# Optimization experiments

Hardware: AMD Instinct MI355X
Metric: run time of the kernel (lower is better)

Reference implementation:

```python
import jax, jax.numpy as jnp
import numpy as np
from jax import lax

WINDOW_SIZE = 11
SIGMA = 1.5
DATA_RANGE = 1.0


def _gaussian_window(channels):
    coords = jnp.arange(WINDOW_SIZE, dtype=jnp.float32) - WINDOW_SIZE // 2
    g = jnp.exp(-coords ** 2 / (2.0 * SIGMA ** 2))
    g = g / g.sum()
    w2d = jnp.outer(g, g)
    w2d = w2d / w2d.sum()
    # depthwise kernel: (C, 1, K, K) in OIHW with feature_group_count=C
    return jnp.broadcast_to(w2d, (channels, 1, WINDOW_SIZE, WINDOW_SIZE))


def _dwconv(x, window, channels):
    pad = WINDOW_SIZE // 2
    return lax.conv_general_dilated(
        x, window,
        window_strides=(1, 1),
        padding=[(pad, pad), (pad, pad)],
        dimension_numbers=('NCHW', 'OIHW', 'NCHW'),
        feature_group_count=channels,
    )


def setup_inputs() -> dict:
    key = jax.random.key(0)
    k1, k2 = jax.random.split(key)
    B, C, H, W = 16, 3, 512, 512
    x = jax.random.uniform(k1, (B, C, H, W), dtype=jnp.float32)
    y = jax.random.uniform(k2, (B, C, H, W), dtype=jnp.float32)
    return {"x": x, "y": y}


def reference(x, y):
    channels = x.shape[1]
    window = _gaussian_window(channels)
    mu_x = _dwconv(x, window, channels)
    mu_y = _dwconv(y, window, channels)
    mu_x2 = mu_x * mu_x
    mu_y2 = mu_y * mu_y
    mu_xy = mu_x * mu_y
    sigma_x2 = _dwconv(x * x, window, channels) - mu_x2
    sigma_y2 = _dwconv(y * y, window, channels) - mu_y2
    sigma_xy = _dwconv(x * y, window, channels) - mu_xy
    c1 = (0.01 * DATA_RANGE) ** 2
    c2 = (0.03 * DATA_RANGE) ** 2
    ssim_map = (2 * mu_xy + c1) * (2 * sigma_xy + c2) / (
        (mu_x2 + mu_y2 + c1) * (sigma_x2 + sigma_y2 + c2) + 1e-08)
    per_image = ssim_map.mean(axis=(1, 2, 3))
    return 1.0 - per_image.mean()
```

## Files before the change

kernel.cpp:

```cpp
#include <hip/hip_runtime.h>
#include <math.h>


#define IMG_W 512
#define IMG_H 512
#define PLANES 48
#define TX 64
#define TY 32
#define RAD 5
#define KW 11
#define NPAIR 21
#define SJ 65
#define NT 256
#define GDX (IMG_W / TX)
#define GDY (IMG_H / TY)
#define NBLK (GDX * GDY * PLANES)

typedef _Float16 h2 __attribute__((ext_vector_type(2)));

#if __has_builtin(__builtin_amdgcn_fdot2)
__device__ __forceinline__ float DOT2(h2 a, h2 b, float c) {
    return __builtin_amdgcn_fdot2(a, b, c, false);
}
#else
__device__ __forceinline__ float DOT2(h2 a, h2 b, float c) {
    return c + (float)a.x * (float)b.x + (float)a.y * (float)b.y;
}
#endif

__device__ __forceinline__ h2 pkrtz(float a, float b) {
    auto t = __builtin_amdgcn_cvt_pkrtz(a, b);
    h2 r;
    __builtin_memcpy(&r, &t, sizeof(r));
    return r;
}

template<bool INTERIOR>
__device__ __forceinline__ void hpass_item(
    int r, int g, int ty0, int bx0,
    const float* __restrict__ xp, const float* __restrict__ yp,
    _Float16* __restrict__ hbh,
    const h2 (* __restrict__ w2)[6])
{
    const int gy = ty0 + r;
    const int j0 = bx0 + g * 8;
    const float4 z4 = make_float4(0.f, 0.f, 0.f, 0.f);

    h2 xh[11], yh[11];
    {
        const bool rowok = INTERIOR || ((unsigned)gy < (unsigned)IMG_H);
        const float* rowx = xp + (size_t)gy * IMG_W;
        const float* rowy = yp + (size_t)gy * IMG_W;
        #pragma unroll
        for (int v = 0; v < 6; ++v) {
            const int gx = j0 - 8 + 4 * v;
            float4 xa, ya;
            if (rowok && (INTERIOR || ((unsigned)gx < (unsigned)IMG_W))) {
                xa = *(const float4*)(rowx + gx);
                ya = *(const float4*)(rowy + gx);
            } else { xa = z4; ya = z4; }
            if (v > 0) {
                xh[2*v] = pkrtz(xa.x, xa.y);
                yh[2*v] = pkrtz(ya.x, ya.y);
            }
            if (v < 5 || true) {
                if (2*v + 1 <= 10) {
                    xh[2*v+1] = pkrtz(xa.z, xa.w);
                    yh[2*v+1] = pkrtz(ya.z, ya.w);
                }
            }
        }
    }

    const int pp = r >> 1, rr = r & 1;
    _Float16* base = hbh + ((pp * 5) * SJ + g * 8) * 2 + rr;
    const int pstr = SJ * 2;

    #pragma unroll
    for (int u = 0; u < 8; ++u) {
        const int t0 = (u + 3) >> 1;
        const h2* wt = w2[(u & 1) ^ 1];
        float fX = 0.f, fY = 0.f;
        #pragma unroll
        for (int q = 0; q < 6; ++q) {
            fX = DOT2(xh[t0 + q], wt[q], fX);
            fY = DOT2(yh[t0 + q], wt[q], fY);
        }
        base[2*u + 0*pstr] = (_Float16)fX;
        base[2*u + 1*pstr] = (_Float16)fY;
    }

    h2 xxh[11], yyh[11], xyh[11];
    #pragma unroll
    for (int t = 1; t <= 10; ++t) {
        xxh[t] = xh[t] * xh[t];
        yyh[t] = yh[t] * yh[t];
        xyh[t] = xh[t] * yh[t];
    }

    #pragma unroll
    for (int u = 0; u < 8; ++u) {
        const int t0 = (u + 3) >> 1;
        const h2* wt = w2[(u & 1) ^ 1];
        float fXX = 0.f, fYY = 0.f, fXY = 0.f;
        #pragma unroll
        for (int q = 0; q < 6; ++q) {
            fXX = DOT2(xxh[t0 + q], wt[q], fXX);
            fYY = DOT2(yyh[t0 + q], wt[q], fYY);
            fXY = DOT2(xyh[t0 + q], wt[q], fXY);
        }
        base[2*u + 2*pstr] = (_Float16)fXX;
        base[2*u + 3*pstr] = (_Float16)fYY;
        base[2*u + 4*pstr] = (_Float16)fXY;
    }
}

__global__ __launch_bounds__(NT, 4) void ssim_tile_kernel(
    const float* __restrict__ x, const float* __restrict__ y,
    float* __restrict__ partials)
{
    __shared__ h2 hb[NPAIR][5][SJ];
    __shared__ float wave_sums[NT / 64];

    float w[KW];
    {
        float s = 0.f;
        #pragma unroll
        for (int k = 0; k < KW; ++k) {
            const float d = (float)(k - RAD);
            w[k] = expf(-d * d * (1.f / (2.f * 1.5f * 1.5f)));
            s += w[k];
        }
        const float inv = 1.f / s;
        #pragma unroll
        for (int k = 0; k < KW; ++k) w[k] *= inv;
    }
    _Float16 wh[KW];
    float cv;
    {
        float s2 = 0.f;
        #pragma unroll
        for (int k = 0; k < KW; ++k) { wh[k] = (_Float16)w[k]; s2 += (float)wh[k]; }
        cv = 1.f / (s2 * s2);
    }
    h2 w2[2][6];
    #pragma unroll
    for (int q = 0; q < 5; ++q) { w2[0][q].x = wh[2*q];   w2[0][q].y = wh[2*q+1]; }
    w2[0][5].x = wh[10]; w2[0][5].y = (_Float16)0.f;
    w2[1][0].x = (_Float16)0.f; w2[1][0].y = wh[0];
    #pragma unroll
    for (int q = 1; q < 6; ++q) { w2[1][q].x = wh[2*q-1]; w2[1][q].y = wh[2*q]; }

    const int tid = threadIdx.x;
    const int plane = blockIdx.z;
    const float* __restrict__ xp = x + (size_t)plane * IMG_H * IMG_W;
    const float* __restrict__ yp = y + (size_t)plane * IMG_H * IMG_W;
    const int bx0 = blockIdx.x * TX;
    const int ty0 = blockIdx.y * TY - RAD;

    const bool interior =
        (bx0 >= 8) && (bx0 + TX + 8 <= IMG_W) &&
        (ty0 >= 0) && (ty0 + 2 * NPAIR <= IMG_H);

    _Float16* hbh = (_Float16*)hb;

    if (interior) {
        hpass_item<true>(tid >> 3, tid & 7, ty0, bx0, xp, yp, hbh, w2);
        if (tid < 42 * 8 - NT)
            hpass_item<true>(32 + (tid >> 3), tid & 7, ty0, bx0, xp, yp, hbh, w2);
    } else {
        hpass_item<false>(tid >> 3, tid & 7, ty0, bx0, xp, yp, hbh, w2);
        if (tid < 42 * 8 - NT)
            hpass_item<false>(32 + (tid >> 3), tid & 7, ty0, bx0, xp, yp, hbh, w2);
    }
    __syncthreads();

    const int j  = tid & 63;
    const int P0 = (tid >> 6) * 4;

    float acc[5][8];
    #pragma unroll
    for (int p = 0; p < 5; ++p)
        #pragma unroll
        for (int u = 0; u < 8; ++u) acc[p][u] = 0.f;

    #pragma unroll
    for (int pp = 0; pp < 9; ++pp) {
        h2 v[5];
        #pragma unroll
        for (int p = 0; p < 5; ++p)
            v[p] = hb[P0 + pp][p][j];
        const int ulo = (2 * pp - 10) > 0 ? (2 * pp - 10) : 0;
        const int uhi = (2 * pp + 1) < 7 ? (2 * pp + 1) : 7;
        #pragma unroll
        for (int u = ulo; u <= uhi; ++u) {
            const h2 wv = w2[u & 1][pp - (u >> 1)];
            #pragma unroll
            for (int p = 0; p < 5; ++p)
                acc[p][u] = DOT2(v[p], wv, acc[p][u]);
        }
    }

    float local = 0.f;
    #pragma unroll
    for (int u = 0; u < 8; ++u) {
        const float mx = acc[0][u] * cv, my = acc[1][u] * cv;
        const float xx = acc[2][u] * cv, yy = acc[3][u] * cv, xy = acc[4][u] * cv;
        const float mx2 = mx * mx, my2 = my * my, mxy = mx * my;
        const float sx2 = xx - mx2, sy2 = yy - my2, sxy = xy - mxy;
        const float c1 = 1e-4f, c2 = 9e-4f;
        const float num = (2.f * mxy + c1) * (2.f * sxy + c2);
        const float den = (mx2 + my2 + c1) * (sx2 + sy2 + c2) + 1e-8f;
        local += num * __builtin_amdgcn_rcpf(den);
    }

    #pragma unroll
    for (int off = 32; off > 0; off >>= 1)
        local += __shfl_down(local, off, 64);
    const int lane = tid & 63, wv = tid >> 6;
    if (lane == 0) wave_sums[wv] = local;
    __syncthreads();
    if (tid == 0) {
        const float s = wave_sums[0] + wave_sums[1] + wave_sums[2] + wave_sums[3];
        const int bid = blockIdx.x + GDX * (blockIdx.y + GDY * blockIdx.z);
        partials[bid] = s;
    }
}

__global__ __launch_bounds__(NT) void ssim_finalize_kernel(
    const float* __restrict__ partials, float* __restrict__ out)
{
    const int tid = threadIdx.x;
    double s = 0.0;
    #pragma unroll 4
    for (int i = tid; i < NBLK; i += NT) s += (double)partials[i];
    #pragma unroll
    for (int off = 32; off > 0; off >>= 1)
        s += __shfl_down(s, off, 64);
    __shared__ double ws_[NT / 64];
    const int lane = tid & 63, wv = tid >> 6;
    if (lane == 0) ws_[wv] = s;
    __syncthreads();
    if (tid == 0) {
        const double t = ws_[0] + ws_[1] + ws_[2] + ws_[3];
        const double n = (double)PLANES * IMG_H * IMG_W;
        out[0] = (float)(1.0 - t / n);
    }
}

extern "C" void kernel_launch(void* const* d_in, const int* in_sizes, int n_in,
                              void* d_out, int out_size, void* d_ws, size_t ws_size,
                              hipStream_t stream)
{
    const float* x = (const float*)d_in[0];
    const float* y = (const float*)d_in[1];
    float* out = (float*)d_out;
    float* partials = (float*)d_ws;

    dim3 grid(GDX, GDY, PLANES);
    ssim_tile_kernel<<<grid, NT, 0, stream>>>(x, y, partials);
    ssim_finalize_kernel<<<1, NT, 0, stream>>>(partials, out);
}
```

Before: 147.0 us.

## Reformulate SSIM moments via sum/difference signals to cut one convolved channel

Replaces the five filtered channels (x, y, x², y², xy) with four: s=x+y, d=x−y, s², d², and recovers the SSIM terms algebraically (2μxμy and 2σxy from the differences of squares). This cuts the horizontal-pass dot products, the shared-memory footprint and the vertical-pass accumulators by about a fifth. The launch-bounds occupancy hint is raised from 4 to 5 to use the freed registers and LDS. The risk is precision: s² is filtered and stored in fp16, and σ is recovered by cancellation between larger fp16 terms, which could loosen accuracy.

```diff
diff --git a/kernel.cpp b/kernel.cpp
--- a/kernel.cpp
+++ b/kernel.cpp
@@ -46,7 +46,7 @@
     const int j0 = bx0 + g * 8;
     const float4 z4 = make_float4(0.f, 0.f, 0.f, 0.f);
 
-    h2 xh[11], yh[11];
+    h2 sh[11], dh[11];
     {
         const bool rowok = INTERIOR || ((unsigned)gy < (unsigned)IMG_H);
         const float* rowx = xp + (size_t)gy * IMG_W;
@@ -59,67 +59,64 @@
                 xa = *(const float4*)(rowx + gx);
                 ya = *(const float4*)(rowy + gx);
             } else { xa = z4; ya = z4; }
-            if (v > 0) {
-                xh[2*v] = pkrtz(xa.x, xa.y);
-                yh[2*v] = pkrtz(ya.x, ya.y);
+            if (2*v >= 1 && 2*v <= 10) {
+                const h2 xh = pkrtz(xa.x, xa.y), yh = pkrtz(ya.x, ya.y);
+                sh[2*v] = xh + yh;
+                dh[2*v] = xh - yh;
             }
-            if (v < 5 || true) {
-                if (2*v + 1 <= 10) {
-                    xh[2*v+1] = pkrtz(xa.z, xa.w);
-                    yh[2*v+1] = pkrtz(ya.z, ya.w);
-                }
+            if (2*v + 1 <= 10) {
+                const h2 xh = pkrtz(xa.z, xa.w), yh = pkrtz(ya.z, ya.w);
+                sh[2*v+1] = xh + yh;
+                dh[2*v+1] = xh - yh;
             }
         }
     }
 
     const int pp = r >> 1, rr = r & 1;
-    _Float16* base = hbh + ((pp * 5) * SJ + g * 8) * 2 + rr;
+    _Float16* base = hbh + ((pp * 4) * SJ + g * 8) * 2 + rr;
     const int pstr = SJ * 2;
 
     #pragma unroll
     for (int u = 0; u < 8; ++u) {
         const int t0 = (u + 3) >> 1;
         const h2* wt = w2[(u & 1) ^ 1];
-        float fX = 0.f, fY = 0.f;
+        float fS = 0.f, fD = 0.f;
         #pragma unroll
         for (int q = 0; q < 6; ++q) {
-            fX = DOT2(xh[t0 + q], wt[q], fX);
-            fY = DOT2(yh[t0 + q], wt[q], fY);
-        }
-        base[2*u + 0*pstr] = (_Float16)fX;
-        base[2*u + 1*pstr] = (_Float16)fY;
-    }
-
-    h2 xxh[11], yyh[11], xyh[11];
+            fS = DOT2(sh[t0 + q], wt[q], fS);
+            fD = DOT2(dh[t0 + q], wt[q], fD);
+        }
+        base[2*u + 0*pstr] = (_Float16)fS;
+        base[2*u + 1*pstr] = (_Float16)fD;
+    }
+
+    h2 s2h[11], d2h[11];
     #pragma unroll
     for (int t = 1; t <= 10; ++t) {
-        xxh[t] = xh[t] * xh[t];
-        yyh[t] = yh[t] * yh[t];
-        xyh[t] = xh[t] * yh[t];
+        s2h[t] = sh[t] * sh[t];
+        d2h[t] = dh[t] * dh[t];
     }
 
     #pragma unroll
     for (int u = 0; u < 8; ++u) {
         const int t0 = (u + 3) >> 1;
         const h2* wt = w2[(u & 1) ^ 1];
-        float fXX = 0.f, fYY = 0.f, fXY = 0.f;
+        float fS2 = 0.f, fD2 = 0.f;
         #pragma unroll
         for (int q = 0; q < 6; ++q) {
-            fXX = DOT2(xxh[t0 + q], wt[q], fXX);
-            fYY = DOT2(yyh[t0 + q], wt[q], fYY);
-            fXY = DOT2(xyh[t0 + q], wt[q], fXY);
-        }
-        base[2*u + 2*pstr] = (_Float16)fXX;
-        base[2*u + 3*pstr] = (_Float16)fYY;
-        base[2*u + 4*pstr] = (_Float16)fXY;
-    }
-}
-
-__global__ __launch_bounds__(NT, 4) void ssim_tile_kernel(
+            fS2 = DOT2(s2h[t0 + q], wt[q], fS2);
+            fD2 = DOT2(d2h[t0 + q], wt[q], fD2);
+        }
+        base[2*u + 2*pstr] = (_Float16)fS2;
+        base[2*u + 3*pstr] = (_Float16)fD2;
+    }
+}
+
+__global__ __launch_bounds__(NT, 5) void ssim_tile_kernel(
     const float* __restrict__ x, const float* __restrict__ y,
     float* __restrict__ partials)
 {
-    __shared__ h2 hb[NPAIR][5][SJ];
+    __shared__ h2 hb[NPAIR][4][SJ];
     __shared__ float wave_sums[NT / 64];
 
     float w[KW];
@@ -178,17 +175,17 @@
     const int j  = tid & 63;
     const int P0 = (tid >> 6) * 4;
 
-    float acc[5][8];
-    #pragma unroll
-    for (int p = 0; p < 5; ++p)
+    float acc[4][8];
+    #pragma unroll
+    for (int p = 0; p < 4; ++p)
         #pragma unroll
         for (int u = 0; u < 8; ++u) acc[p][u] = 0.f;
 
     #pragma unroll
     for (int pp = 0; pp < 9; ++pp) {
-        h2 v[5];
-        #pragma unroll
-        for (int p = 0; p < 5; ++p)
+        h2 v[4];
+        #pragma unroll
+        for (int p = 0; p < 4; ++p)
             v[p] = hb[P0 + pp][p][j];
         const int ulo = (2 * pp - 10) > 0 ? (2 * pp - 10) : 0;
         const int uhi = (2 * pp + 1) < 7 ? (2 * pp + 1) : 7;
@@ -196,7 +193,7 @@
         for (int u = ulo; u <= uhi; ++u) {
             const h2 wv = w2[u & 1][pp - (u >> 1)];
             #pragma unroll
-            for (int p = 0; p < 5; ++p)
+            for (int p = 0; p < 4; ++p)
                 acc[p][u] = DOT2(v[p], wv, acc[p][u]);
         }
     }
@@ -204,13 +201,16 @@
     float local = 0.f;
     #pragma unroll
     for (int u = 0; u < 8; ++u) {
-        const float mx = acc[0][u] * cv, my = acc[1][u] * cv;
-        const float xx = acc[2][u] * cv, yy = acc[3][u] * cv, xy = acc[4][u] * cv;
-        const float mx2 = mx * mx, my2 = my * my, mxy = mx * my;
-        const float sx2 = xx - mx2, sy2 = yy - my2, sxy = xy - mxy;
+        const float mS = acc[0][u] * cv, mD = acc[1][u] * cv;
+        const float eS = acc[2][u] * cv, eD = acc[3][u] * cv;
+        const float ms2 = mS * mS, md2 = mD * mD;
+        const float Pm = 0.5f * (ms2 - md2);
+        const float Qm = 0.5f * (ms2 + md2);
+        const float Pe = 0.5f * (eS - eD);
+        const float Qe = 0.5f * (eS + eD);
         const float c1 = 1e-4f, c2 = 9e-4f;
-        const float num = (2.f * mxy + c1) * (2.f * sxy + c2);
-        const float den = (mx2 + my2 + c1) * (sx2 + sy2 + c2) + 1e-8f;
+        const float num = (Pm + c1) * (Pe - Pm + c2);
+        const float den = (Qm + c1) * (Qe - Qm + c2) + 1e-8f;
         local += num * __builtin_amdgcn_rcpf(den);
     }
 
```

Result: no change. 144.2 us (-1.9%).
